# Kernel optimization log

Measured on AMD Instinct MI355X. Metric: run time of the kernel, lower is better.

The kernel has to match this reference:

```python
import jax, jax.numpy as jnp
import numpy as np

DIM = 512
NUM_EXPERTS = 8
HID = 4 * DIM
B, S = 2, 2048


def setup_inputs() -> dict:
    key = jax.random.key(0)
    ks = jax.random.split(key, 7)
    sc = 0.02
    x = jax.random.normal(ks[0], (B, S, DIM), dtype=jnp.float32)
    Wr = jax.random.normal(ks[1], (DIM, NUM_EXPERTS), dtype=jnp.float32) * sc
    br = jnp.zeros((NUM_EXPERTS,), dtype=jnp.float32)
    W1 = jax.random.normal(ks[2], (NUM_EXPERTS, DIM, HID), dtype=jnp.float32) * sc
    b1 = jnp.zeros((NUM_EXPERTS, HID), dtype=jnp.float32)
    W2 = jax.random.normal(ks[3], (NUM_EXPERTS, HID, DIM), dtype=jnp.float32) * sc
    b2 = jnp.zeros((NUM_EXPERTS, DIM), dtype=jnp.float32)
    return {"x": x, "Wr": Wr, "br": br, "W1": W1, "b1": b1, "W2": W2, "b2": b2}


def reference(x, Wr, br, W1, b1, W2, b2):
    b, s, d = x.shape
    E = Wr.shape[1]
    xf = x.reshape(-1, d)                                   # [N, d]
    N = xf.shape[0]
    logits = xf @ Wr + br                                   # [N, E]
    probs = jax.nn.softmax(logits, axis=-1)
    top_w, top_idx = jax.lax.top_k(probs, 2)                # [N, 2]
    top_w = jax.nn.softmax(top_w, axis=-1)                  # renormalize top-2
    # combine weight per (token, expert); topk indices are distinct so add is safe
    comb = jnp.zeros((N, E), dtype=xf.dtype)
    comb = comb.at[jnp.arange(N)[:, None], top_idx].add(top_w)  # [N, E]
    # dense per-expert MLP (eval mode: dropout is identity); exact GELU as nn.GELU
    h = jax.nn.gelu(jnp.einsum('nd,edf->enf', xf, W1) + b1[:, None, :], approximate=False)
    y = jnp.einsum('enf,efd->end', h, W2) + b2[:, None, :]  # [E, N, d]
    out = jnp.einsum('end,ne->nd', y, comb)                 # weighted combine
    # load-balancing loss
    load = jnp.zeros((E,), dtype=jnp.float32).at[top_idx.reshape(-1)].add(1.0)
    load = load / load.sum()
    lb_loss = jnp.sum((load - 1.0 / E) ** 2)
    return out.reshape(b, s, d), lb_loss, load
```

## Files before the change

kernel.cpp:

```cpp
#include <hip/hip_runtime.h>
#include <hip/hip_bf16.h>

#define DIMD 512
#define NEXP 8
#define HIDN 2048
#define NTOK 4096
#define NASG 8192

typedef short bf16x8 __attribute__((ext_vector_type(8)));
typedef float f32x4 __attribute__((ext_vector_type(4)));

__device__ inline unsigned short f2bf(float f) {
  __hip_bfloat16 h = __float2bfloat16(f);
  return __builtin_bit_cast(unsigned short, h);
}

__device__ inline void gl16(const void* g, void* l) {
  __builtin_amdgcn_global_load_lds(
      (const __attribute__((address_space(1))) unsigned int*)g,
      (__attribute__((address_space(3))) unsigned int*)l, 16, 0, 0);
}

#define PIPE_WAIT4_BAR() do { \
  asm volatile("s_waitcnt vmcnt(4)" ::: "memory"); \
  __builtin_amdgcn_s_barrier(); \
  __builtin_amdgcn_sched_barrier(0); } while (0)
#define PIPE_WAIT0_BAR() do { \
  asm volatile("s_waitcnt vmcnt(0)" ::: "memory"); \
  __builtin_amdgcn_s_barrier(); \
  __builtin_amdgcn_sched_barrier(0); } while (0)
#define PIPE_POST_BAR() do { \
  asm volatile("" ::: "memory"); \
  __builtin_amdgcn_sched_barrier(0); \
  __builtin_amdgcn_s_barrier(); } while (0)

__global__ __launch_bounds__(256) void transpose_both_kernel(
    const float* __restrict__ W1, const float* __restrict__ W2,
    unsigned short* __restrict__ w1t, unsigned short* __restrict__ w2t) {
  __shared__ float tile[64][65];
  int z = blockIdx.z;
  int e = z & 7;
  const float* src; unsigned short* dst; int R, C, r0, c0;
  if (z < 8) { src = W1; dst = w1t; R = DIMD; C = HIDN; c0 = blockIdx.x * 64; r0 = blockIdx.y * 64; }
  else       { src = W2; dst = w2t; R = HIDN; C = DIMD; r0 = blockIdx.x * 64; c0 = blockIdx.y * 64; }
  const float* s = src + (size_t)e * R * C;
  unsigned short* d = dst + (size_t)e * R * C;
  for (int i = threadIdx.x; i < 1024; i += 256) {
    int r = i >> 4, c4 = (i & 15) * 4;
    float4 v = *reinterpret_cast<const float4*>(s + (size_t)(r0 + r) * C + (c0 + c4));
    tile[r][c4] = v.x; tile[r][c4 + 1] = v.y; tile[r][c4 + 2] = v.z; tile[r][c4 + 3] = v.w;
  }
  __syncthreads();
  for (int i = threadIdx.x; i < 1024; i += 256) {
    int c = i >> 4;
    int r = (i & 15) * 4;
    unsigned u0 = (unsigned)f2bf(tile[r][c]) | ((unsigned)f2bf(tile[r + 1][c]) << 16);
    unsigned u1 = (unsigned)f2bf(tile[r + 2][c]) | ((unsigned)f2bf(tile[r + 3][c]) << 16);
    *reinterpret_cast<uint2*>(d + (size_t)(c0 + c) * R + (r0 + r)) = make_uint2(u0, u1);
  }
}

__global__ __launch_bounds__(256) void router_kernel(const float* __restrict__ x,
                                                     const float* __restrict__ Wr,
                                                     const float* __restrict__ br,
                                                     int* __restrict__ tidx,
                                                     float* __restrict__ tw,
                                                     unsigned short* __restrict__ xb) {
  int lane = threadIdx.x & 63;
  int n = blockIdx.x * 4 + (threadIdx.x >> 6);
  const float* xr = x + (size_t)n * DIMD;
  unsigned short* xbr = xb + (size_t)n * DIMD;
  int d0 = lane * 8;
  float4 xa = *reinterpret_cast<const float4*>(xr + d0);
  float4 xc = *reinterpret_cast<const float4*>(xr + d0 + 4);
  uint4 pk;
  pk.x = (unsigned)f2bf(xa.x) | ((unsigned)f2bf(xa.y) << 16);
  pk.y = (unsigned)f2bf(xa.z) | ((unsigned)f2bf(xa.w) << 16);
  pk.z = (unsigned)f2bf(xc.x) | ((unsigned)f2bf(xc.y) << 16);
  pk.w = (unsigned)f2bf(xc.z) | ((unsigned)f2bf(xc.w) << 16);
  *reinterpret_cast<uint4*>(xbr + d0) = pk;

  float acc[NEXP];
#pragma unroll
  for (int e = 0; e < NEXP; ++e) acc[e] = 0.f;
  const float* wr = Wr + (size_t)d0 * NEXP;
#pragma unroll
  for (int j = 0; j < 8; ++j) {
    float xj = (j < 4) ? (&xa.x)[j] : (&xc.x)[j - 4];
    float4 w0 = *reinterpret_cast<const float4*>(wr + j * NEXP);
    float4 w1 = *reinterpret_cast<const float4*>(wr + j * NEXP + 4);
    acc[0] += xj * w0.x; acc[1] += xj * w0.y; acc[2] += xj * w0.z; acc[3] += xj * w0.w;
    acc[4] += xj * w1.x; acc[5] += xj * w1.y; acc[6] += xj * w1.z; acc[7] += xj * w1.w;
  }
#pragma unroll
  for (int e = 0; e < NEXP; ++e) {
    float v = acc[e];
#pragma unroll
    for (int off = 32; off > 0; off >>= 1) v += __shfl_xor(v, off, 64);
    acc[e] = v + br[e];
  }
  if (lane == 0) {
    float m = acc[0];
    for (int e = 1; e < NEXP; ++e) m = fmaxf(m, acc[e]);
    float p[NEXP], s = 0.f;
    for (int e = 0; e < NEXP; ++e) { p[e] = expf(acc[e] - m); s += p[e]; }
    float inv = 1.f / s;
    for (int e = 0; e < NEXP; ++e) p[e] *= inv;
    int i0 = 0; float p0 = p[0];
    for (int e = 1; e < NEXP; ++e) if (p[e] > p0) { p0 = p[e]; i0 = e; }
    int i1 = (i0 == 0) ? 1 : 0; float p1 = p[i1];
    for (int e = 0; e < NEXP; ++e) if (e != i0 && p[e] > p1) { p1 = p[e]; i1 = e; }
    float t = expf(p1 - p0);
    float w0 = 1.f / (1.f + t);
    tidx[2 * n] = i0; tidx[2 * n + 1] = i1;
    tw[2 * n] = w0; tw[2 * n + 1] = t * w0;
  }
}

__global__ __launch_bounds__(1024) void route_pack_kernel(const int* __restrict__ tidx,
                                                          int* __restrict__ off,
                                                          int* __restrict__ list,
                                                          float* __restrict__ out_tail) {
  int tid = threadIdx.x;
  int wv = tid >> 6, lane = tid & 63;

  int ids[8];
#pragma unroll
  for (int j = 0; j < 8; ++j) ids[j] = tidx[tid * 8 + j];

  int c[NEXP];
#pragma unroll
  for (int e = 0; e < NEXP; ++e) c[e] = 0;
#pragma unroll
  for (int j = 0; j < 8; ++j)
#pragma unroll
    for (int e = 0; e < NEXP; ++e) c[e] += (ids[j] == e) ? 1 : 0;

  int inc[NEXP];
#pragma unroll
  for (int e = 0; e < NEXP; ++e) {
    int v = c[e];
#pragma unroll
    for (int d = 1; d < 64; d <<= 1) {
      int t = __shfl_up(v, d, 64);
      if (lane >= d) v += t;
    }
    inc[e] = v;
  }

  __shared__ int wtot[NEXP][16];
  __shared__ int wbase[NEXP][16];
  __shared__ int ebase[NEXP];
  if (lane == 63) {
#pragma unroll
    for (int e = 0; e < NEXP; ++e) wtot[e][wv] = inc[e];
  }
  __syncthreads();
  if (tid < NEXP) {
    int e = tid;
    int s = 0;
#pragma unroll
    for (int w = 0; w < 16; ++w) { wbase[e][w] = s; s += wtot[e][w]; }
    int pfx = s;
#pragma unroll
    for (int d = 1; d < 8; d <<= 1) {
      int t = __shfl_up(pfx, d, 64);
      if (tid >= d) pfx += t;
    }
    int base = pfx - s;
    ebase[e] = base;
    off[e] = base;
    if (e == NEXP - 1) off[NEXP] = pfx;
    float l = (float)s / (float)NASG;
    out_tail[1 + e] = l;
    float dd = l - 0.125f;
    float lb = dd * dd;
#pragma unroll
    for (int d = 1; d < 8; d <<= 1) lb += __shfl_xor(lb, d, 64);
    if (e == 0) out_tail[0] = lb;
  }
  __syncthreads();

  int pos[NEXP];
#pragma unroll
  for (int e = 0; e < NEXP; ++e)
    pos[e] = ebase[e] + wbase[e][wv] + (inc[e] - c[e]);

#pragma unroll
  for (int j = 0; j < 8; ++j) {
    int e = ids[j];
    int p = 0;
#pragma unroll
    for (int k = 0; k < NEXP; ++k)
      if (e == k) { p = pos[k]; pos[k] = p + 1; }
    list[p] = tid * 8 + j;
  }
}


__global__ __launch_bounds__(256) void gemm1_kernel(
    const unsigned short* __restrict__ xb,
    const unsigned short* __restrict__ w1t,
    const float* __restrict__ b1,
    const int* __restrict__ off,
    const int* __restrict__ list,
    unsigned short* __restrict__ H) {
  int e = blockIdx.x;
  int offe = off[e];
  int cnt_e = off[e + 1] - offe;
  int n0 = blockIdx.y * 128;
  int m0 = blockIdx.z * 128;
  if (m0 >= cnt_e) return;

  __shared__ char ldsb[36864];

  int tid = threadIdx.x, wv = tid >> 6, lane = tid & 63;
  int rp = lane >> 3, sl = lane & 7;
  int sx = sl ^ rp;
  int rowadd = rp * 2 + (sx >> 2);
  int kq = sx & 3;

  const unsigned short* w1e = w1t + (size_t)e * HIDN * DIMD;
  const unsigned short* asrc[2];
  const unsigned short* bsrc[2];
#pragma unroll
  for (int i = 0; i < 2; ++i) {
    int r = wv * 32 + i * 16 + rowadd;
    int rr = m0 + r;
    int tok = 0;
    if (rr < cnt_e) tok = list[offe + rr] >> 1;
    asrc[i] = xb + (size_t)tok * DIMD + kq * 8;
    bsrc[i] = w1e + (size_t)(n0 + r) * DIMD + kq * 8;
  }
  int dstA0 = wv * 2048;
  int dstA1 = wv * 2048 + 1024;

  f32x4 zero = {0.f, 0.f, 0.f, 0.f};
  f32x4 acc[4][4];
#pragma unroll
  for (int m = 0; m < 4; ++m)
#pragma unroll
    for (int n = 0; n < 4; ++n) acc[m][n] = zero;

  int wave_m = wv >> 1, wave_n = wv & 1;
  int lane16 = lane & 15, kq4 = lane >> 4;
  int ra[4], rb[4];
#pragma unroll
  for (int m = 0; m < 4; ++m) {
    int r = wave_m * 64 + m * 16 + lane16;
    ra[m] = (r >> 1) * 128 + ((((kq4 + (r & 1) * 4)) ^ ((r >> 1) & 7)) << 4);
    int rn = wave_n * 64 + m * 16 + lane16;
    rb[m] = (rn >> 1) * 128 + ((((kq4 + (rn & 1) * 4)) ^ ((rn >> 1) & 7)) << 4);
  }

  auto stage = [&](char* nb, int k0) {
    gl16(asrc[0] + k0, nb + dstA0);
    gl16(asrc[1] + k0, nb + dstA1);
    gl16(bsrc[0] + k0, nb + 8192 + dstA0);
    gl16(bsrc[1] + k0, nb + 8192 + dstA1);
  };
  auto compute = [&](const char* cb) {
    bf16x8 af[4], bfr[4];
#pragma unroll
    for (int m = 0; m < 4; ++m) af[m] = *reinterpret_cast<const bf16x8*>(cb + ra[m]);
#pragma unroll
    for (int n = 0; n < 4; ++n) bfr[n] = *reinterpret_cast<const bf16x8*>(cb + 8192 + rb[n]);
#pragma unroll
    for (int m = 0; m < 4; ++m)
#pragma unroll
      for (int n = 0; n < 4; ++n)
        acc[m][n] = __builtin_amdgcn_mfma_f32_16x16x32_bf16(af[m], bfr[n], acc[m][n], 0, 0, 0);
  };

  const int T = DIMD / 32;
  stage(ldsb, 0);
  stage(ldsb + 16384, 32);
  for (int t = 0; t < T - 2; ++t) {
    char* cb = ldsb + (t & 1) * 16384;
    PIPE_WAIT4_BAR();
    compute(cb);
    PIPE_POST_BAR();
    stage(cb, (t + 2) * 32);
  }
  PIPE_WAIT4_BAR();
  compute(ldsb + ((T - 2) & 1) * 16384);
  PIPE_POST_BAR();
  PIPE_WAIT0_BAR();
  compute(ldsb + ((T - 1) & 1) * 16384);
  PIPE_POST_BAR();

  unsigned short* Ct = (unsigned short*)ldsb;
  const float* b1e = b1 + e * HIDN;
#pragma unroll
  for (int n = 0; n < 4; ++n) {
    int cl = wave_n * 64 + n * 16 + lane16;
    float bias = b1e[n0 + cl];
#pragma unroll
    for (int m = 0; m < 4; ++m) {
#pragma unroll
      for (int q = 0; q < 4; ++q) {
        int rl = wave_m * 64 + m * 16 + kq4 * 4 + q;
        float v = acc[m][n][q] + bias;
        float g = 0.5f * v * (1.f + erff(v * 0.70710678118654752f));
        Ct[rl * 136 + cl] = f2bf(g);
      }
    }
  }
  __syncthreads();
  for (int u = tid; u < 2048; u += 256) {
    int rl = u >> 4, c8 = (u & 15) * 8;
    int r = m0 + rl;
    if (r < cnt_e) {
      uint4 v = *reinterpret_cast<const uint4*>(Ct + rl * 136 + c8);
      *reinterpret_cast<uint4*>(H + (size_t)(offe + r) * HIDN + n0 + c8) = v;
    }
  }
}

__global__ __launch_bounds__(256) void gemm2_kernel(
    const unsigned short* __restrict__ H,
    const unsigned short* __restrict__ w2t,
    const float* __restrict__ b2,
    const int* __restrict__ off,
    const int* __restrict__ list,
    const float* __restrict__ tw,
    float* __restrict__ Yw) {
  int e = blockIdx.x;
  int offe = off[e];
  int cnt_e = off[e + 1] - offe;
  int n0 = blockIdx.y * 128;
  int m0 = blockIdx.z * 128;
  if (m0 >= cnt_e) return;

  __shared__ char ldsb[32768];

  int tid = threadIdx.x, wv = tid >> 6, lane = tid & 63;
  int rp = lane >> 3, sl = lane & 7;
  int sx = sl ^ rp;
  int rowadd = rp * 2 + (sx >> 2);
  int kq = sx & 3;

  const unsigned short* w2e = w2t + (size_t)e * DIMD * HIDN;
  const unsigned short* asrc[2];
  const unsigned short* bsrc[2];
#pragma unroll
  for (int i = 0; i < 2; ++i) {
    int r = wv * 32 + i * 16 + rowadd;
    int rowa = offe + m0 + r;
    if (rowa > NASG - 1) rowa = NASG - 1;
    asrc[i] = H + (size_t)rowa * HIDN + kq * 8;
    bsrc[i] = w2e + (size_t)(n0 + r) * HIDN + kq * 8;
  }
  int dstA0 = wv * 2048;
  int dstA1 = wv * 2048 + 1024;

  f32x4 zero = {0.f, 0.f, 0.f, 0.f};
  f32x4 acc[4][4];
#pragma unroll
  for (int m = 0; m < 4; ++m)
#pragma unroll
    for (int n = 0; n < 4; ++n) acc[m][n] = zero;

  int wave_m = wv >> 1, wave_n = wv & 1;
  int lane16 = lane & 15, kq4 = lane >> 4;
  int ra[4], rb[4];
#pragma unroll
  for (int m = 0; m < 4; ++m) {
    int r = wave_m * 64 + m * 16 + lane16;
    ra[m] = (r >> 1) * 128 + ((((kq4 + (r & 1) * 4)) ^ ((r >> 1) & 7)) << 4);
    int rn = wave_n * 64 + m * 16 + lane16;
    rb[m] = (rn >> 1) * 128 + ((((kq4 + (rn & 1) * 4)) ^ ((rn >> 1) & 7)) << 4);
  }

  auto stage = [&](char* nb, int k0) {
    gl16(asrc[0] + k0, nb + dstA0);
    gl16(asrc[1] + k0, nb + dstA1);
    gl16(bsrc[0] + k0, nb + 8192 + dstA0);
    gl16(bsrc[1] + k0, nb + 8192 + dstA1);
  };
  auto compute = [&](const char* cb) {
    bf16x8 af[4], bfr[4];
#pragma unroll
    for (int m = 0; m < 4; ++m) af[m] = *reinterpret_cast<const bf16x8*>(cb + ra[m]);
#pragma unroll
    for (int n = 0; n < 4; ++n) bfr[n] = *reinterpret_cast<const bf16x8*>(cb + 8192 + rb[n]);
#pragma unroll
    for (int m = 0; m < 4; ++m)
#pragma unroll
      for (int n = 0; n < 4; ++n)
        acc[m][n] = __builtin_amdgcn_mfma_f32_16x16x32_bf16(af[m], bfr[n], acc[m][n], 0, 0, 0);
  };

  const int T = HIDN / 32;
  stage(ldsb, 0);
  stage(ldsb + 16384, 32);
  for (int t = 0; t < T - 2; ++t) {
    char* cb = ldsb + (t & 1) * 16384;
    PIPE_WAIT4_BAR();
    compute(cb);
    PIPE_POST_BAR();
    stage(cb, (t + 2) * 32);
  }
  PIPE_WAIT4_BAR();
  compute(ldsb + ((T - 2) & 1) * 16384);
  PIPE_POST_BAR();
  PIPE_WAIT0_BAR();
  compute(ldsb + ((T - 1) & 1) * 16384);
  PIPE_POST_BAR();

  const float* b2e = b2 + e * DIMD;
  float bias[4];
#pragma unroll
  for (int n = 0; n < 4; ++n) bias[n] = b2e[n0 + wave_n * 64 + n * 16 + lane16];
#pragma unroll
  for (int m = 0; m < 4; ++m) {
#pragma unroll
    for (int q = 0; q < 4; ++q) {
      int r = m0 + wave_m * 64 + m * 16 + kq4 * 4 + q;
      if (r < cnt_e) {
        int a = list[offe + r];
        float w = tw[a];
        float* yrow = Yw + (size_t)a * DIMD;
#pragma unroll
        for (int n = 0; n < 4; ++n) {
          int col = n0 + wave_n * 64 + n * 16 + lane16;
          yrow[col] = w * (acc[m][n][q] + bias[n]);
        }
      }
    }
  }
}

__global__ __launch_bounds__(256) void combine_kernel(const float* __restrict__ Yw,
                                                      float* __restrict__ out) {
  int i = (blockIdx.x * 256 + threadIdx.x) * 4;
  int n = i >> 9;
  int d = i & 511;
  float4 a = *reinterpret_cast<const float4*>(Yw + (size_t)(2 * n) * DIMD + d);
  float4 b = *reinterpret_cast<const float4*>(Yw + (size_t)(2 * n + 1) * DIMD + d);
  float4 o;
  o.x = a.x + b.x; o.y = a.y + b.y; o.z = a.z + b.z; o.w = a.w + b.w;
  *reinterpret_cast<float4*>(out + i) = o;
}

extern "C" void kernel_launch(void* const* d_in, const int* in_sizes, int n_in,
                              void* d_out, int out_size, void* d_ws, size_t ws_size,
                              hipStream_t stream) {
  const float* x  = (const float*)d_in[0];
  const float* Wr = (const float*)d_in[1];
  const float* br = (const float*)d_in[2];
  const float* W1 = (const float*)d_in[3];
  const float* b1 = (const float*)d_in[4];
  const float* W2 = (const float*)d_in[5];
  const float* b2 = (const float*)d_in[6];
  float* out = (float*)d_out;

  char* ws = (char*)d_ws;
  unsigned short* xb  = (unsigned short*)ws;  ws += (size_t)NTOK * DIMD * 2;
  unsigned short* w1t = (unsigned short*)ws;  ws += (size_t)NEXP * HIDN * DIMD * 2;
  unsigned short* w2t = (unsigned short*)ws;  ws += (size_t)NEXP * DIMD * HIDN * 2;
  unsigned short* H   = (unsigned short*)ws;  ws += (size_t)NASG * HIDN * 2;
  float* Yw = (float*)ws;                     ws += (size_t)NASG * DIMD * 4;
  float* tw = (float*)ws;                     ws += (size_t)NASG * 4;
  int* tidx = (int*)ws;                       ws += (size_t)NASG * 4;
  int* list = (int*)ws;                       ws += (size_t)NASG * 4;
  int* offp = (int*)ws;

  transpose_both_kernel<<<dim3(32, 8, 16), 256, 0, stream>>>(W1, W2, w1t, w2t);
  router_kernel<<<NTOK / 4, 256, 0, stream>>>(x, Wr, br, tidx, tw, xb);
  route_pack_kernel<<<1, 1024, 0, stream>>>(tidx, offp, list, out + (size_t)NTOK * DIMD);
  gemm1_kernel<<<dim3(NEXP, HIDN / 128, NASG / 128), 256, 0, stream>>>(xb, w1t, b1, offp, list, H);
  gemm2_kernel<<<dim3(NEXP, DIMD / 128, NASG / 128), 256, 0, stream>>>(H, w2t, b2, offp, list, tw, Yw);
  combine_kernel<<<2048, 256, 0, stream>>>(Yw, out);
}
```

Before: 117.1 us.

## Give each wave private LDS tiles to drop block barriers in GEMM pipelines

Each of the four waves now stages its own 64-row A and B slices into a private LDS region, so the K-loop no longer needs workgroup barriers. Only per-wave vmcnt/lgkmcnt waits order the loads and the double buffering. This removes barrier stalls between waves, but each wave now fetches A and B rows that were shared across waves before, so global/L2 traffic doubles. LDS use also grows to 64 KB per block, which may reduce occupancy.

```diff
diff --git a/kernel.cpp b/kernel.cpp
--- a/kernel.cpp
+++ b/kernel.cpp
@@ -21,18 +21,15 @@
       (__attribute__((address_space(3))) unsigned int*)l, 16, 0, 0);
 }
 
-#define PIPE_WAIT4_BAR() do { \
-  asm volatile("s_waitcnt vmcnt(4)" ::: "memory"); \
-  __builtin_amdgcn_s_barrier(); \
+#define VM_WAIT8() do { \
+  asm volatile("s_waitcnt vmcnt(8)" ::: "memory"); \
   __builtin_amdgcn_sched_barrier(0); } while (0)
-#define PIPE_WAIT0_BAR() do { \
+#define VM_WAIT0() do { \
   asm volatile("s_waitcnt vmcnt(0)" ::: "memory"); \
-  __builtin_amdgcn_s_barrier(); \
   __builtin_amdgcn_sched_barrier(0); } while (0)
-#define PIPE_POST_BAR() do { \
-  asm volatile("" ::: "memory"); \
-  __builtin_amdgcn_sched_barrier(0); \
-  __builtin_amdgcn_s_barrier(); } while (0)
+#define LGKM_FENCE() do { \
+  asm volatile("s_waitcnt lgkmcnt(0)" ::: "memory"); \
+  __builtin_amdgcn_sched_barrier(0); } while (0)
 
 __global__ __launch_bounds__(256) void transpose_both_kernel(
     const float* __restrict__ W1, const float* __restrict__ W2,
@@ -212,28 +209,28 @@
   int m0 = blockIdx.z * 128;
   if (m0 >= cnt_e) return;
 
-  __shared__ char ldsb[36864];
+  __shared__ char ldsb[65536];
 
   int tid = threadIdx.x, wv = tid >> 6, lane = tid & 63;
   int rp = lane >> 3, sl = lane & 7;
   int sx = sl ^ rp;
   int rowadd = rp * 2 + (sx >> 2);
   int kq = sx & 3;
+  int wave_m = wv >> 1, wave_n = wv & 1;
+  int wb = wv * 16384;
 
   const unsigned short* w1e = w1t + (size_t)e * HIDN * DIMD;
-  const unsigned short* asrc[2];
-  const unsigned short* bsrc[2];
-#pragma unroll
-  for (int i = 0; i < 2; ++i) {
-    int r = wv * 32 + i * 16 + rowadd;
-    int rr = m0 + r;
+  const unsigned short* aptr[4];
+  const unsigned short* bptr[4];
+#pragma unroll
+  for (int i = 0; i < 4; ++i) {
+    int rA = m0 + wave_m * 64 + i * 16 + rowadd;
     int tok = 0;
-    if (rr < cnt_e) tok = list[offe + rr] >> 1;
-    asrc[i] = xb + (size_t)tok * DIMD + kq * 8;
-    bsrc[i] = w1e + (size_t)(n0 + r) * DIMD + kq * 8;
-  }
-  int dstA0 = wv * 2048;
-  int dstA1 = wv * 2048 + 1024;
+    if (rA < cnt_e) tok = list[offe + rA] >> 1;
+    aptr[i] = xb + (size_t)tok * DIMD + kq * 8;
+    int rB = n0 + wave_n * 64 + i * 16 + rowadd;
+    bptr[i] = w1e + (size_t)rB * DIMD + kq * 8;
+  }
 
   f32x4 zero = {0.f, 0.f, 0.f, 0.f};
   f32x4 acc[4][4];
@@ -242,52 +239,50 @@
 #pragma unroll
     for (int n = 0; n < 4; ++n) acc[m][n] = zero;
 
-  int wave_m = wv >> 1, wave_n = wv & 1;
   int lane16 = lane & 15, kq4 = lane >> 4;
   int ra[4], rb[4];
 #pragma unroll
   for (int m = 0; m < 4; ++m) {
-    int r = wave_m * 64 + m * 16 + lane16;
+    int r = m * 16 + lane16;
     ra[m] = (r >> 1) * 128 + ((((kq4 + (r & 1) * 4)) ^ ((r >> 1) & 7)) << 4);
-    int rn = wave_n * 64 + m * 16 + lane16;
-    rb[m] = (rn >> 1) * 128 + ((((kq4 + (rn & 1) * 4)) ^ ((rn >> 1) & 7)) << 4);
-  }
-
-  auto stage = [&](char* nb, int k0) {
-    gl16(asrc[0] + k0, nb + dstA0);
-    gl16(asrc[1] + k0, nb + dstA1);
-    gl16(bsrc[0] + k0, nb + 8192 + dstA0);
-    gl16(bsrc[1] + k0, nb + 8192 + dstA1);
+    rb[m] = ra[m];
+  }
+
+  auto stage = [&](int d, int k0) {
+    char* A = ldsb + wb + d * 8192;
+    char* B = A + 4096;
+    gl16(aptr[0] + k0, A);
+    gl16(aptr[1] + k0, A + 1024);
+    gl16(aptr[2] + k0, A + 2048);
+    gl16(aptr[3] + k0, A + 3072);
+    gl16(bptr[0] + k0, B);
+    gl16(bptr[1] + k0, B + 1024);
+    gl16(bptr[2] + k0, B + 2048);
+    gl16(bptr[3] + k0, B + 3072);
   };
-  auto compute = [&](const char* cb) {
+
+  const int T = DIMD / 32;
+  stage(0, 0);
+  stage(1, 32);
+  for (int t = 0; t < T; ++t) {
+    const char* A = ldsb + wb + (t & 1) * 8192;
+    const char* B = A + 4096;
+    if (t < T - 1) { VM_WAIT8(); } else { VM_WAIT0(); }
     bf16x8 af[4], bfr[4];
 #pragma unroll
-    for (int m = 0; m < 4; ++m) af[m] = *reinterpret_cast<const bf16x8*>(cb + ra[m]);
-#pragma unroll
-    for (int n = 0; n < 4; ++n) bfr[n] = *reinterpret_cast<const bf16x8*>(cb + 8192 + rb[n]);
+    for (int m = 0; m < 4; ++m) af[m] = *reinterpret_cast<const bf16x8*>(A + ra[m]);
+#pragma unroll
+    for (int n = 0; n < 4; ++n) bfr[n] = *reinterpret_cast<const bf16x8*>(B + rb[n]);
+    LGKM_FENCE();
+    if (t + 2 < T) stage(t & 1, (t + 2) * 32);
+    __builtin_amdgcn_sched_barrier(0);
 #pragma unroll
     for (int m = 0; m < 4; ++m)
 #pragma unroll
       for (int n = 0; n < 4; ++n)
         acc[m][n] = __builtin_amdgcn_mfma_f32_16x16x32_bf16(af[m], bfr[n], acc[m][n], 0, 0, 0);
-  };
-
-  const int T = DIMD / 32;
-  stage(ldsb, 0);
-  stage(ldsb + 16384, 32);
-  for (int t = 0; t < T - 2; ++t) {
-    char* cb = ldsb + (t & 1) * 16384;
-    PIPE_WAIT4_BAR();
-    compute(cb);
-    PIPE_POST_BAR();
-    stage(cb, (t + 2) * 32);
-  }
-  PIPE_WAIT4_BAR();
-  compute(ldsb + ((T - 2) & 1) * 16384);
-  PIPE_POST_BAR();
-  PIPE_WAIT0_BAR();
-  compute(ldsb + ((T - 1) & 1) * 16384);
-  PIPE_POST_BAR();
+  }
+  __syncthreads();
 
   unsigned short* Ct = (unsigned short*)ldsb;
   const float* b1e = b1 + e * HIDN;
@@ -332,27 +327,27 @@
   int m0 = blockIdx.z * 128;
   if (m0 >= cnt_e) return;
 
-  __shared__ char ldsb[32768];
+  __shared__ char ldsb[65536];
 
   int tid = threadIdx.x, wv = tid >> 6, lane = tid & 63;
   int rp = lane >> 3, sl = lane & 7;
   int sx = sl ^ rp;
   int rowadd = rp * 2 + (sx >> 2);
   int kq = sx & 3;
+  int wave_m = wv >> 1, wave_n = wv & 1;
+  int wb = wv * 16384;
 
   const unsigned short* w2e = w2t + (size_t)e * DIMD * HIDN;
-  const unsigned short* asrc[2];
-  const unsigned short* bsrc[2];
-#pragma unroll
-  for (int i = 0; i < 2; ++i) {
-    int r = wv * 32 + i * 16 + rowadd;
-    int rowa = offe + m0 + r;
-    if (rowa > NASG - 1) rowa = NASG - 1;
-    asrc[i] = H + (size_t)rowa * HIDN + kq * 8;
-    bsrc[i] = w2e + (size_t)(n0 + r) * HIDN + kq * 8;
-  }
-  int dstA0 = wv * 2048;
-  int dstA1 = wv * 2048 + 1024;
+  const unsigned short* aptr[4];
+  const unsigned short* bptr[4];
+#pragma unroll
+  for (int i = 0; i < 4; ++i) {
+    int rA = offe + m0 + wave_m * 64 + i * 16 + rowadd;
+    if (rA > NASG - 1) rA = NASG - 1;
+    aptr[i] = H + (size_t)rA * HIDN + kq * 8;
+    int rB = n0 + wave_n * 64 + i * 16 + rowadd;
+    bptr[i] = w2e + (size_t)rB * HIDN + kq * 8;
+  }
 
   f32x4 zero = {0.f, 0.f, 0.f, 0.f};
   f32x4 acc[4][4];
@@ -361,52 +356,49 @@
 #pragma unroll
     for (int n = 0; n < 4; ++n) acc[m][n] = zero;
 
-  int wave_m = wv >> 1, wave_n = wv & 1;
   int lane16 = lane & 15, kq4 = lane >> 4;
   int ra[4], rb[4];
 #pragma unroll
   for (int m = 0; m < 4; ++m) {
-    int r = wave_m * 64 + m * 16 + lane16;
+    int r = m * 16 + lane16;
     ra[m] = (r >> 1) * 128 + ((((kq4 + (r & 1) * 4)) ^ ((r >> 1) & 7)) << 4);
-    int rn = wave_n * 64 + m * 16 + lane16;
-    rb[m] = (rn >> 1) * 128 + ((((kq4 + (rn & 1) * 4)) ^ ((rn >> 1) & 7)) << 4);
-  }
-
-  auto stage = [&](char* nb, int k0) {
-    gl16(asrc[0] + k0, nb + dstA0);
-    gl16(asrc[1] + k0, nb + dstA1);
-    gl16(bsrc[0] + k0, nb + 8192 + dstA0);
-    gl16(bsrc[1] + k0, nb + 8192 + dstA1);
+    rb[m] = ra[m];
+  }
+
+  auto stage = [&](int d, int k0) {
+    char* A = ldsb + wb + d * 8192;
+    char* B = A + 4096;
+    gl16(aptr[0] + k0, A);
+    gl16(aptr[1] + k0, A + 1024);
+    gl16(aptr[2] + k0, A + 2048);
+    gl16(aptr[3] + k0, A + 3072);
+    gl16(bptr[0] + k0, B);
+    gl16(bptr[1] + k0, B + 1024);
+    gl16(bptr[2] + k0, B + 2048);
+    gl16(bptr[3] + k0, B + 3072);
   };
-  auto compute = [&](const char* cb) {
+
+  const int T = HIDN / 32;
+  stage(0, 0);
+  stage(1, 32);
+  for (int t = 0; t < T; ++t) {
+    const char* A = ldsb + wb + (t & 1) * 8192;
+    const char* B = A + 4096;
+    if (t < T - 1) { VM_WAIT8(); } else { VM_WAIT0(); }
     bf16x8 af[4], bfr[4];
 #pragma unroll
-    for (int m = 0; m < 4; ++m) af[m] = *reinterpret_cast<const bf16x8*>(cb + ra[m]);
-#pragma unroll
-    for (int n = 0; n < 4; ++n) bfr[n] = *reinterpret_cast<const bf16x8*>(cb + 8192 + rb[n]);
+    for (int m = 0; m < 4; ++m) af[m] = *reinterpret_cast<const bf16x8*>(A + ra[m]);
+#pragma unroll
+    for (int n = 0; n < 4; ++n) bfr[n] = *reinterpret_cast<const bf16x8*>(B + rb[n]);
+    LGKM_FENCE();
+    if (t + 2 < T) stage(t & 1, (t + 2) * 32);
+    __builtin_amdgcn_sched_barrier(0);
 #pragma unroll
     for (int m = 0; m < 4; ++m)
 #pragma unroll
       for (int n = 0; n < 4; ++n)
         acc[m][n] = __builtin_amdgcn_mfma_f32_16x16x32_bf16(af[m], bfr[n], acc[m][n], 0, 0, 0);
-  };
-
-  const int T = HIDN / 32;
-  stage(ldsb, 0);
-  stage(ldsb + 16384, 32);
-  for (int t = 0; t < T - 2; ++t) {
-    char* cb = ldsb + (t & 1) * 16384;
-    PIPE_WAIT4_BAR();
-    compute(cb);
-    PIPE_POST_BAR();
-    stage(cb, (t + 2) * 32);
-  }
-  PIPE_WAIT4_BAR();
-  compute(ldsb + ((T - 2) & 1) * 16384);
-  PIPE_POST_BAR();
-  PIPE_WAIT0_BAR();
-  compute(ldsb + ((T - 1) & 1) * 16384);
-  PIPE_POST_BAR();
+  }
 
   const float* b2e = b2 + e * DIMD;
   float bias[4];
```

Result: slower. 140.4 us (+19.9%).
